# Performance work log

Hardware: AMD Instinct MI355X
Metric: run time of the kernel (lower is better)

## Reference

```python
import jax, jax.numpy as jnp
import numpy as np

NUM_PARTS = 16
NUM_K = 256          # num_k_per_part; table rows per part = NUM_K + 1
VAE_DIMS = 768
OUT_DIMS = 1024
B = 4096


def setup_inputs() -> dict:
    key = jax.random.key(0)
    k0, k1, k2, k3, k4 = jax.random.split(key, 5)
    hashes = jax.random.randint(k0, (B, NUM_PARTS), 0, NUM_K + 1)  # values 0..256
    # nn.init.normal_(embedding.weight, 0.0, 0.01)
    emb = jax.random.normal(k1, ((NUM_K + 1) * NUM_PARTS, VAE_DIMS), dtype=jnp.float32) * 0.01
    # projection: Linear(768 -> 1024), ReLU, Linear(1024 -> 1024)
    W1 = jax.random.normal(k2, (VAE_DIMS, OUT_DIMS), dtype=jnp.float32) * (1.0 / np.sqrt(VAE_DIMS))
    b1 = jnp.zeros((OUT_DIMS,), dtype=jnp.float32)
    W2 = jax.random.normal(k3, (OUT_DIMS, OUT_DIMS), dtype=jnp.float32) * (1.0 / np.sqrt(OUT_DIMS))
    b2 = jnp.zeros((OUT_DIMS,), dtype=jnp.float32)
    # pe = randn(num_parts, out_dims) * 1.0
    pe = jax.random.normal(k4, (NUM_PARTS, OUT_DIMS), dtype=jnp.float32)
    return {"hashes": hashes, "emb": emb, "W1": W1, "b1": b1, "W2": W2, "b2": b2, "pe": pe}


def reference(hashes, emb, W1, b1, W2, b2, pe):
    # forward(hashes, index=None, get_mu=False, input_is_mu=False)
    offset = jnp.arange(NUM_PARTS, dtype=hashes.dtype) * (NUM_K + 1)  # [P]
    idx = hashes + offset[None, :]                                    # [B, P]
    mu = emb[idx]                                                     # [B, P, VAE]
    h = jax.nn.relu(jnp.einsum('bpv,vh->bph', mu, W1) + b1)           # [B, P, OUT]
    projected = jnp.einsum('bph,ho->bpo', h, W2) + b2                 # [B, P, OUT]
    return projected + pe[None, :, :]                                 # pe broadcast over batch
```

## Files before the change

### kernel.cpp

```cpp
#include <hip/hip_runtime.h>
#include <stdint.h>

#define NPARTS 16
#define NK1    257
#define ROWS   4112
#define MPAD   4224
#define VAE    768
#define ODIM   1024
#define BROWS  65536

typedef __attribute__((ext_vector_type(4))) float f32x4;
typedef __attribute__((ext_vector_type(8))) short s16x8;

static __device__ __forceinline__ unsigned short f2bf(float f) {
  union { float f; unsigned u; } v; v.f = f;
  unsigned x = v.u;
  unsigned r = x + 0x7FFFu + ((x >> 16) & 1u);
  return (unsigned short)(r >> 16);
}

static __device__ __forceinline__ void gload_lds16(const void* g, void* l) {
  __builtin_amdgcn_global_load_lds(
      (const __attribute__((address_space(1))) unsigned int*)g,
      (__attribute__((address_space(3))) unsigned int*)l, 16, 0, 0);
}

#define EMB_BLOCKS 1024
__global__ __launch_bounds__(256) void prep_kernel(
    const float* __restrict__ emb, const float* __restrict__ W1,
    const float* __restrict__ W2, unsigned short* __restrict__ embB,
    unsigned short* __restrict__ w1t, unsigned short* __restrict__ w2t) {
  __shared__ unsigned short tile[32][33];
  const int tid = threadIdx.x;
  const int bid = blockIdx.x;
  if (bid < EMB_BLOCKS) {
    const int NQ = MPAD * VAE / 4;
    for (int g = bid * 256 + tid; g < NQ; g += EMB_BLOCKS * 256) {
      const int i4 = g * 4;
      ushort4 o;
      if (i4 < ROWS * VAE) {
        const float4 v = *(const float4*)(emb + i4);
        o.x = f2bf(v.x); o.y = f2bf(v.y); o.z = f2bf(v.z); o.w = f2bf(v.w);
      } else {
        o.x = 0; o.y = 0; o.z = 0; o.w = 0;
      }
      *(ushort4*)(embB + i4) = o;
    }
  } else {
    int tb = bid - EMB_BLOCKS;
    const float* W; unsigned short* outp; int KD;
    if (tb < 768) { W = W1; outp = w1t; KD = VAE; }
    else          { tb -= 768; W = W2; outp = w2t; KD = ODIM; }
    const int nkt = KD / 32;
    const int tk = (tb % nkt) * 32;
    const int tn = (tb / nkt) * 32;
    const int r  = tid >> 3;
    const int c4 = (tid & 7) * 4;
    const float4 v = *(const float4*)(W + (size_t)(tk + r) * ODIM + tn + c4);
    tile[r][c4 + 0] = f2bf(v.x);
    tile[r][c4 + 1] = f2bf(v.y);
    tile[r][c4 + 2] = f2bf(v.z);
    tile[r][c4 + 3] = f2bf(v.w);
    __syncthreads();
    ushort4 o;
    o.x = tile[c4 + 0][r];
    o.y = tile[c4 + 1][r];
    o.z = tile[c4 + 2][r];
    o.w = tile[c4 + 3][r];
    *(ushort4*)(outp + (size_t)(tn + r) * KD + tk + c4) = o;
  }
}

template <int K, bool FUSE1>
__global__ __launch_bounds__(256) void gemm_kernel(
    const unsigned short* __restrict__ A, const unsigned short* __restrict__ BT,
    const float* __restrict__ bias, const float* __restrict__ pe,
    unsigned short* __restrict__ outB, float* __restrict__ outF) {
  __shared__ __align__(16) unsigned short As[64 * 32];
  __shared__ __align__(16) unsigned short Bs[128 * 32];

  const int tid  = threadIdx.x;
  const int lane = tid & 63;
  const int wave = tid >> 6;
  const int wc   = wave * 32;
  const int brow = blockIdx.y * 64;
  const int bcol = blockIdx.x * 128;

  f32x4 acc[4][2];
#pragma unroll
  for (int m = 0; m < 4; ++m)
#pragma unroll
    for (int n = 0; n < 2; ++n)
#pragma unroll
      for (int r = 0; r < 4; ++r) acc[m][n][r] = 0.f;

  const int sr = tid >> 2;
  const int sk = (tid & 3) * 8;
  const unsigned short* gA = A + (size_t)(brow + sr) * K + sk;
  const unsigned short* gB = BT + (size_t)(bcol + sr) * K + sk;
  unsigned short* lA = As + sr * 32 + sk;
  unsigned short* lB = Bs + sr * 32 + sk;

  const int la = lane & 15;
  const int lk = (lane >> 4) * 8;

  for (int kt = 0; kt < K; kt += 32) {
    gload_lds16(gA + kt, lA);
    gload_lds16(gB + kt, lB);
    gload_lds16(gB + kt + (size_t)64 * K, lB + 64 * 32);
    __syncthreads();

    s16x8 af[4], bfr[2];
#pragma unroll
    for (int m = 0; m < 4; ++m)
      af[m] = *(const s16x8*)(As + (m * 16 + la) * 32 + lk);
#pragma unroll
    for (int n = 0; n < 2; ++n)
      bfr[n] = *(const s16x8*)(Bs + (wc + n * 16 + la) * 32 + lk);
#pragma unroll
    for (int m = 0; m < 4; ++m)
#pragma unroll
      for (int n = 0; n < 2; ++n)
        acc[m][n] = __builtin_amdgcn_mfma_f32_16x16x32_bf16(af[m], bfr[n], acc[m][n], 0, 0, 0);
    __syncthreads();
  }

#pragma unroll
  for (int m = 0; m < 4; ++m) {
    const int row0 = brow + m * 16 + (lane >> 4) * 4;
#pragma unroll
    for (int n = 0; n < 2; ++n) {
      const int col = bcol + wc + n * 16 + la;
      const float bv = bias[col];
      if (FUSE1) {
#pragma unroll
        for (int r = 0; r < 4; ++r) {
          float v = acc[m][n][r] + bv;
          v = v > 0.f ? v : 0.f;
          outB[(size_t)(row0 + r) * ODIM + col] = f2bf(v);
        }
      } else {
#pragma unroll
        for (int r = 0; r < 4; ++r) {
          const int row = row0 + r;
          int p = row / NK1;
          if (p > NPARTS - 1) p = NPARTS - 1;
          outF[(size_t)row * ODIM + col] = acc[m][n][r] + bv + pe[(size_t)p * ODIM + col];
        }
      }
    }
  }
}

__global__ __launch_bounds__(256) void gather_kernel(const int* __restrict__ hashes,
                                                     const float* __restrict__ T,
                                                     float* __restrict__ out) {
  const int wid  = (blockIdx.x * blockDim.x + threadIdx.x) >> 6;
  const int lane = threadIdx.x & 63;
  const int nw   = (gridDim.x * blockDim.x) >> 6;
  for (int row = wid; row < BROWS; row += nw) {
    const int h = __builtin_amdgcn_readfirstlane(hashes[row]);
    const int p = row & (NPARTS - 1);
    const f32x4* __restrict__ src = (const f32x4*)(T + (size_t)(h + p * NK1) * ODIM);
    f32x4* __restrict__ dst = (f32x4*)(out + (size_t)row * ODIM);
#pragma unroll
    for (int j = 0; j < 4; ++j) {
      f32x4 v = src[lane + j * 64];
      __builtin_nontemporal_store(v, dst + lane + j * 64);
    }
  }
}

extern "C" void kernel_launch(void* const* d_in, const int* in_sizes, int n_in,
                              void* d_out, int out_size, void* d_ws, size_t ws_size,
                              hipStream_t stream) {
  const int*   hashes = (const int*)d_in[0];
  const float* emb    = (const float*)d_in[1];
  const float* W1     = (const float*)d_in[2];
  const float* b1     = (const float*)d_in[3];
  const float* W2     = (const float*)d_in[4];
  const float* b2     = (const float*)d_in[5];
  const float* pe     = (const float*)d_in[6];
  float* out = (float*)d_out;

  char* ws = (char*)d_ws;
  unsigned short* embB = (unsigned short*)(ws);
  unsigned short* w1t  = (unsigned short*)(ws + 6488064);
  unsigned short* w2t  = (unsigned short*)(ws + 8060928);
  unsigned short* H    = (unsigned short*)(ws + 10158080);
  float*          T    = (float*)(ws + 18808832);

  prep_kernel<<<EMB_BLOCKS + 768 + 1024, 256, 0, stream>>>(emb, W1, W2, embB, w1t, w2t);

  dim3 gg(ODIM / 128, MPAD / 64);
  gemm_kernel<VAE, true><<<gg, 256, 0, stream>>>(embB, w1t, b1, nullptr, H, nullptr);
  gemm_kernel<ODIM, false><<<gg, 256, 0, stream>>>(H, w2t, b2, pe, nullptr, T);

  gather_kernel<<<1024, 256, 0, stream>>>(hashes, T, out);
}
```

Baseline: 101.7 us.

## Double-buffer GEMM K-tiles with swizzled LDS and overlap W2 transpose with GEMM1

The GEMM now loads 64-wide K tiles into two LDS buffers, so the next tile's global-to-LDS copy runs while MFMAs consume the current one. The LDS layout uses an XOR swizzle to cut bank conflicts on fragment reads. The W2 bf16 transpose moves out of the prep kernel into extra z-slice blocks of the first GEMM launch, so it runs alongside GEMM1. In exchange, LDS use per block rises, which may lower occupancy.

```diff
diff --git a/kernel.cpp b/kernel.cpp
--- a/kernel.cpp
+++ b/kernel.cpp
@@ -28,8 +28,7 @@
 #define EMB_BLOCKS 1024
 __global__ __launch_bounds__(256) void prep_kernel(
     const float* __restrict__ emb, const float* __restrict__ W1,
-    const float* __restrict__ W2, unsigned short* __restrict__ embB,
-    unsigned short* __restrict__ w1t, unsigned short* __restrict__ w2t) {
+    unsigned short* __restrict__ embB, unsigned short* __restrict__ w1t) {
   __shared__ unsigned short tile[32][33];
   const int tid = threadIdx.x;
   const int bid = blockIdx.x;
@@ -47,16 +46,13 @@
       *(ushort4*)(embB + i4) = o;
     }
   } else {
-    int tb = bid - EMB_BLOCKS;
-    const float* W; unsigned short* outp; int KD;
-    if (tb < 768) { W = W1; outp = w1t; KD = VAE; }
-    else          { tb -= 768; W = W2; outp = w2t; KD = ODIM; }
-    const int nkt = KD / 32;
+    const int tb = bid - EMB_BLOCKS;
+    const int nkt = VAE / 32;
     const int tk = (tb % nkt) * 32;
     const int tn = (tb / nkt) * 32;
     const int r  = tid >> 3;
     const int c4 = (tid & 7) * 4;
-    const float4 v = *(const float4*)(W + (size_t)(tk + r) * ODIM + tn + c4);
+    const float4 v = *(const float4*)(W1 + (size_t)(tk + r) * ODIM + tn + c4);
     tile[r][c4 + 0] = f2bf(v.x);
     tile[r][c4 + 1] = f2bf(v.y);
     tile[r][c4 + 2] = f2bf(v.z);
@@ -67,24 +63,49 @@
     o.y = tile[c4 + 1][r];
     o.z = tile[c4 + 2][r];
     o.w = tile[c4 + 3][r];
-    *(ushort4*)(outp + (size_t)(tn + r) * KD + tk + c4) = o;
-  }
-}
-
-template <int K, bool FUSE1>
+    *(ushort4*)(w1t + (size_t)(tn + r) * VAE + tk + c4) = o;
+  }
+}
+
+template <int K, int MODE, bool DO_W2T>
 __global__ __launch_bounds__(256) void gemm_kernel(
     const unsigned short* __restrict__ A, const unsigned short* __restrict__ BT,
     const float* __restrict__ bias, const float* __restrict__ pe,
-    unsigned short* __restrict__ outB, float* __restrict__ outF) {
-  __shared__ __align__(16) unsigned short As[64 * 32];
-  __shared__ __align__(16) unsigned short Bs[128 * 32];
-
-  const int tid  = threadIdx.x;
+    unsigned short* __restrict__ outB, float* __restrict__ outF,
+    const float* __restrict__ W2src, unsigned short* __restrict__ w2dst) {
+  __shared__ __align__(16) unsigned short smem[2 * 12288];
+  const int tid = threadIdx.x;
+
+  if (DO_W2T && blockIdx.z == 1) {
+    if (blockIdx.y >= 32) return;
+    unsigned short (*tile)[132] = (unsigned short (*)[132])smem;
+    const int tk = blockIdx.y * 32, tn = blockIdx.x * 128;
+#pragma unroll
+    for (int p = 0; p < 4; ++p) {
+      const int row = (tid >> 5) + p * 8, c4 = (tid & 31) * 4;
+      const float4 v = *(const float4*)(W2src + (size_t)(tk + row) * ODIM + tn + c4);
+      tile[row][c4 + 0] = f2bf(v.x); tile[row][c4 + 1] = f2bf(v.y);
+      tile[row][c4 + 2] = f2bf(v.z); tile[row][c4 + 3] = f2bf(v.w);
+    }
+    __syncthreads();
+#pragma unroll
+    for (int q = 0; q < 4; ++q) {
+      const int n = (tid >> 3) + q * 32, k4 = (tid & 7) * 4;
+      ushort4 o;
+      o.x = tile[k4 + 0][n]; o.y = tile[k4 + 1][n];
+      o.z = tile[k4 + 2][n]; o.w = tile[k4 + 3][n];
+      *(ushort4*)(w2dst + (size_t)(tn + n) * ODIM + tk + k4) = o;
+    }
+    return;
+  }
+
   const int lane = tid & 63;
   const int wave = tid >> 6;
   const int wc   = wave * 32;
   const int brow = blockIdx.y * 64;
   const int bcol = blockIdx.x * 128;
+  const int la   = lane & 15;
+  const int hi   = lane >> 4;
 
   f32x4 acc[4][2];
 #pragma unroll
@@ -94,45 +115,69 @@
 #pragma unroll
       for (int r = 0; r < 4; ++r) acc[m][n][r] = 0.f;
 
-  const int sr = tid >> 2;
-  const int sk = (tid & 3) * 8;
-  const unsigned short* gA = A + (size_t)(brow + sr) * K + sk;
-  const unsigned short* gB = BT + (size_t)(bcol + sr) * K + sk;
-  unsigned short* lA = As + sr * 32 + sk;
-  unsigned short* lB = Bs + sr * 32 + sk;
-
-  const int la = lane & 15;
-  const int lk = (lane >> 4) * 8;
-
-  for (int kt = 0; kt < K; kt += 32) {
-    gload_lds16(gA + kt, lA);
-    gload_lds16(gB + kt, lB);
-    gload_lds16(gB + kt + (size_t)64 * K, lB + 64 * 32);
-    __syncthreads();
-
-    s16x8 af[4], bfr[2];
+  const int srow = tid >> 3;
+  const int skb  = (tid & 7) ^ (srow & 7);
+  const unsigned short* gA = A + (size_t)(brow + srow) * K + skb * 8;
+  const unsigned short* gB = BT + (size_t)(bcol + srow) * K + skb * 8;
+
+#define STAGE(b, kt)                                              \
+  {                                                               \
+    unsigned short* la_ = smem + (b) * 12288 + tid * 8;           \
+    unsigned short* lb_ = la_ + 4096;                             \
+    gload_lds16(gA + (kt), la_);                                  \
+    gload_lds16(gA + (kt) + 32 * K, la_ + 2048);                  \
+    gload_lds16(gB + (kt), lb_);                                  \
+    gload_lds16(gB + (kt) + 32 * K, lb_ + 2048);                  \
+    gload_lds16(gB + (kt) + 64 * K, lb_ + 4096);                  \
+    gload_lds16(gB + (kt) + 96 * K, lb_ + 6144);                  \
+  }
+
+  STAGE(0, 0);
+  asm volatile("s_waitcnt vmcnt(0)" ::: "memory");
+  __builtin_amdgcn_s_barrier();
+
+  const int NT = K / 64;
+  for (int t = 0; t < NT; ++t) {
+    const int cur = t & 1;
+    if (t + 1 < NT) STAGE(cur ^ 1, (t + 1) * 64);
+
+    const unsigned short* As = smem + cur * 12288;
+    const unsigned short* Bs = As + 4096;
+    s16x8 af[4][2], bf[2][2];
 #pragma unroll
     for (int m = 0; m < 4; ++m)
-      af[m] = *(const s16x8*)(As + (m * 16 + la) * 32 + lk);
+#pragma unroll
+      for (int ks = 0; ks < 2; ++ks)
+        af[m][ks] = *(const s16x8*)(As + (m * 16 + la) * 64 +
+                                    (((ks * 4 + hi) ^ (la & 7)) * 8));
 #pragma unroll
     for (int n = 0; n < 2; ++n)
-      bfr[n] = *(const s16x8*)(Bs + (wc + n * 16 + la) * 32 + lk);
+#pragma unroll
+      for (int ks = 0; ks < 2; ++ks)
+        bf[n][ks] = *(const s16x8*)(Bs + (wc + n * 16 + la) * 64 +
+                                    (((ks * 4 + hi) ^ (la & 7)) * 8));
 #pragma unroll
     for (int m = 0; m < 4; ++m)
 #pragma unroll
       for (int n = 0; n < 2; ++n)
-        acc[m][n] = __builtin_amdgcn_mfma_f32_16x16x32_bf16(af[m], bfr[n], acc[m][n], 0, 0, 0);
-    __syncthreads();
-  }
+#pragma unroll
+        for (int ks = 0; ks < 2; ++ks)
+          acc[m][n] = __builtin_amdgcn_mfma_f32_16x16x32_bf16(af[m][ks], bf[n][ks],
+                                                              acc[m][n], 0, 0, 0);
+    asm volatile("s_waitcnt vmcnt(0)" ::: "memory");
+    __builtin_amdgcn_sched_barrier(0);
+    __builtin_amdgcn_s_barrier();
+  }
+#undef STAGE
 
 #pragma unroll
   for (int m = 0; m < 4; ++m) {
-    const int row0 = brow + m * 16 + (lane >> 4) * 4;
+    const int row0 = brow + m * 16 + hi * 4;
 #pragma unroll
     for (int n = 0; n < 2; ++n) {
       const int col = bcol + wc + n * 16 + la;
       const float bv = bias[col];
-      if (FUSE1) {
+      if (MODE == 0) {
 #pragma unroll
         for (int r = 0; r < 4; ++r) {
           float v = acc[m][n][r] + bv;
@@ -190,11 +235,13 @@
   unsigned short* H    = (unsigned short*)(ws + 10158080);
   float*          T    = (float*)(ws + 18808832);
 
-  prep_kernel<<<EMB_BLOCKS + 768 + 1024, 256, 0, stream>>>(emb, W1, W2, embB, w1t, w2t);
-
-  dim3 gg(ODIM / 128, MPAD / 64);
-  gemm_kernel<VAE, true><<<gg, 256, 0, stream>>>(embB, w1t, b1, nullptr, H, nullptr);
-  gemm_kernel<ODIM, false><<<gg, 256, 0, stream>>>(H, w2t, b2, pe, nullptr, T);
+  prep_kernel<<<EMB_BLOCKS + 768, 256, 0, stream>>>(emb, W1, embB, w1t);
+
+  gemm_kernel<VAE, 0, true><<<dim3(8, 66, 2), 256, 0, stream>>>(
+      embB, w1t, b1, nullptr, H, nullptr, W2, w2t);
+
+  gemm_kernel<ODIM, 2, false><<<dim3(8, 66, 1), 256, 0, stream>>>(
+      H, w2t, b2, pe, nullptr, T, nullptr, nullptr);
 
   gather_kernel<<<1024, 256, 0, stream>>>(hashes, T, out);
 }
```

Result: faster. 94.00 us (-7.6%).
